# Kernel optimization log

Measured on AMD Instinct MI355X. Metric: run time of the kernel, lower is better.

## Reference

```python
import jax, jax.numpy as jnp
import numpy as np

OUT_H, OUT_W = 7, 7  # output_size from init_kwargs


def setup_inputs() -> dict:
    key = jax.random.key(0)
    k1, k2 = jax.random.split(key)
    B, C, H, W = 2, 256, 200, 304
    N = 512  # proposals per image
    feature_map = jax.random.normal(k1, (B, C, H, W), dtype=jnp.float32)
    u = jax.random.uniform(k2, (B, N, 5), dtype=jnp.float32)
    # [cx, cy, w, h, angle_deg] in image coordinates
    boxes = jnp.stack([
        u[..., 0] * W,            # cx in [0, W)
        u[..., 1] * H,            # cy in [0, H)
        16.0 + u[..., 2] * 100.0, # w in [16, 116)
        16.0 + u[..., 3] * 100.0, # h in [16, 116)
        u[..., 4] * 360.0,        # angle in degrees
    ], axis=-1)
    return {"feature_map": feature_map, "boxes": boxes}


def _make_grid(boxes, H, W):
    # boxes: [B, N, 5] -> normalized sampling grid (gx, gy) each [B, N, OUT_H, OUT_W]
    cx, cy, w, h, ang = (boxes[..., i] for i in range(5))
    rad = -ang * (jnp.pi / 180.0)
    c, s = jnp.cos(rad), jnp.sin(rad)
    a00 = w / W * c
    a01 = -h / H * s
    a02 = 2.0 * cx / W - 1.0
    a10 = w / W * s
    a11 = h / H * c
    a12 = 2.0 * cy / H - 1.0
    # affine_grid base coords, align_corners=False
    xs = (2.0 * jnp.arange(OUT_W, dtype=boxes.dtype) + 1.0) / OUT_W - 1.0  # [OUT_W]
    ys = (2.0 * jnp.arange(OUT_H, dtype=boxes.dtype) + 1.0) / OUT_H - 1.0  # [OUT_H]
    xs = xs[None, None, None, :]
    ys = ys[None, None, :, None]
    gx = a00[..., None, None] * xs + a01[..., None, None] * ys + a02[..., None, None]
    gy = a10[..., None, None] * xs + a11[..., None, None] * ys + a12[..., None, None]
    return gx, gy


def _sample_one_image(fm, ix, iy):
    # fm: [C, H, W]; ix, iy: [N, OUT_H, OUT_W] pixel coords. Bilinear, zero padding.
    H, W = fm.shape[1], fm.shape[2]
    x0 = jnp.floor(ix)
    y0 = jnp.floor(iy)
    wx1 = ix - x0
    wy1 = iy - y0

    def corner(yc, xc, wgt):
        valid = (xc >= 0) & (xc <= W - 1) & (yc >= 0) & (yc <= H - 1)
        xi = jnp.clip(xc, 0, W - 1).astype(jnp.int32)
        yi = jnp.clip(yc, 0, H - 1).astype(jnp.int32)
        vals = fm[:, yi, xi]  # [C, N, OUT_H, OUT_W]
        return vals * (wgt * valid)[None]

    out = (corner(y0, x0, (1 - wy1) * (1 - wx1))
           + corner(y0, x0 + 1, (1 - wy1) * wx1)
           + corner(y0 + 1, x0, wy1 * (1 - wx1))
           + corner(y0 + 1, x0 + 1, wy1 * wx1))
    return jnp.transpose(out, (1, 0, 2, 3))  # [N, C, OUT_H, OUT_W]


def reference(feature_map, boxes):
    B, C, H, W = feature_map.shape
    N = boxes.shape[1]
    gx, gy = _make_grid(boxes, H, W)  # normalized [-1, 1]
    # grid_sample align_corners=False coordinate transform
    ix = ((gx + 1.0) * W - 1.0) * 0.5
    iy = ((gy + 1.0) * H - 1.0) * 0.5
    pooled = jax.vmap(_sample_one_image)(feature_map, ix, iy)  # [B, N, C, OUT_H, OUT_W]
    return pooled.reshape(B * N, C, OUT_H, OUT_W)
```

## Files before the change

kernel.cpp:

```cpp
#include <hip/hip_runtime.h>
#include <hip/hip_fp16.h>

#define B_   2
#define C_   256
#define H_   200
#define W_   304
#define HW_  60800
#define N_   512
#define OH_  7
#define OW_  7
#define POS_ 49
#define CPB_ 12544
#define PD_  258

__global__ __launch_bounds__(256) void transpose_f16_kernel(
    const float* __restrict__ fm,
    __half* __restrict__ fmT)
{
    __shared__ float tile[64 * 65];

    const int blk = blockIdx.x;
    const int b   = blk / 3800;
    const int r   = blk - b * 3800;
    const int hwT = r >> 2;
    const int cT  = r & 3;
    const int hw0 = hwT * 64;
    const int c0  = cT * 64;

    const int t      = threadIdx.x;
    const int lane16 = t & 15;
    const int grp    = t >> 4;

    const float* src = fm + ((size_t)b * C_ + c0) * HW_ + hw0;

    #pragma unroll
    for (int p = 0; p < 4; ++p) {
        const int c_local = p * 16 + grp;
        const float4 v = *(const float4*)(src + (size_t)c_local * HW_ + lane16 * 4);
        float* dl = &tile[c_local * 65 + lane16 * 4];
        dl[0] = v.x; dl[1] = v.y; dl[2] = v.z; dl[3] = v.w;
    }
    __syncthreads();

    __half* dst = fmT + ((size_t)b * HW_ + hw0) * C_ + c0;

    #pragma unroll
    for (int p = 0; p < 4; ++p) {
        const int hw_local = p * 16 + grp;
        ushort4 u;
        u.x = __half_as_ushort(__float2half_rn(tile[(lane16 * 4 + 0) * 65 + hw_local]));
        u.y = __half_as_ushort(__float2half_rn(tile[(lane16 * 4 + 1) * 65 + hw_local]));
        u.z = __half_as_ushort(__float2half_rn(tile[(lane16 * 4 + 2) * 65 + hw_local]));
        u.w = __half_as_ushort(__float2half_rn(tile[(lane16 * 4 + 3) * 65 + hw_local]));
        *(ushort4*)(dst + (size_t)hw_local * C_ + lane16 * 4) = u;
    }
}

__global__ __launch_bounds__(256) void gather_f16_kernel(
    const __half* __restrict__ fmT,
    const float* __restrict__ boxes,
    float* __restrict__ out)
{
    __shared__ int4   sOff[POS_];
    __shared__ float4 sWgt[POS_];
    __shared__ float  sVal[48 * PD_ + 256];

    const int bn  = blockIdx.x;
    const int b   = bn >> 9;
    const int tid = threadIdx.x;

    if (tid < POS_) {
        const float* bx = boxes + (size_t)bn * 5;
        const float cx = bx[0], cy = bx[1], w = bx[2], h = bx[3], ang = bx[4];

        const float rad = -ang * 0.017453292519943295f;
        const float cr = cosf(rad), sr = sinf(rad);

        const float a00 =  w * (1.0f / W_) * cr;
        const float a01 = -h * (1.0f / H_) * sr;
        const float a02 =  2.0f * cx * (1.0f / W_) - 1.0f;
        const float a10 =  w * (1.0f / W_) * sr;
        const float a11 =  h * (1.0f / H_) * cr;
        const float a12 =  2.0f * cy * (1.0f / H_) - 1.0f;

        const int py = tid / OW_;
        const int px = tid - py * OW_;
        const float xs = (2.0f * (float)px + 1.0f) / (float)OW_ - 1.0f;
        const float ys = (2.0f * (float)py + 1.0f) / (float)OH_ - 1.0f;

        const float gx = a00 * xs + a01 * ys + a02;
        const float gy = a10 * xs + a11 * ys + a12;

        const float ix = ((gx + 1.0f) * (float)W_ - 1.0f) * 0.5f;
        const float iy = ((gy + 1.0f) * (float)H_ - 1.0f) * 0.5f;

        const float x0f = floorf(ix), y0f = floorf(iy);
        const float wx1 = ix - x0f,  wy1 = iy - y0f;
        const float wx0 = 1.0f - wx1, wy0 = 1.0f - wy1;
        const float x1f = x0f + 1.0f, y1f = y0f + 1.0f;

        const float vx0 = (x0f >= 0.0f && x0f <= (float)(W_ - 1)) ? 1.0f : 0.0f;
        const float vx1 = (x1f >= 0.0f && x1f <= (float)(W_ - 1)) ? 1.0f : 0.0f;
        const float vy0 = (y0f >= 0.0f && y0f <= (float)(H_ - 1)) ? 1.0f : 0.0f;
        const float vy1 = (y1f >= 0.0f && y1f <= (float)(H_ - 1)) ? 1.0f : 0.0f;

        const int xi0 = (int)fminf(fmaxf(x0f, 0.0f), (float)(W_ - 1));
        const int xi1 = (int)fminf(fmaxf(x1f, 0.0f), (float)(W_ - 1));
        const int yi0 = (int)fminf(fmaxf(y0f, 0.0f), (float)(H_ - 1));
        const int yi1 = (int)fminf(fmaxf(y1f, 0.0f), (float)(H_ - 1));

        sOff[tid] = make_int4((yi0 * W_ + xi0) * C_, (yi0 * W_ + xi1) * C_,
                              (yi1 * W_ + xi0) * C_, (yi1 * W_ + xi1) * C_);
        sWgt[tid] = make_float4(wy0 * wx0 * (vy0 * vx0),
                                wy0 * wx1 * (vy0 * vx1),
                                wy1 * wx0 * (vy1 * vx0),
                                wy1 * wx1 * (vy1 * vx1));
    }
    __syncthreads();

    const int t128 = tid & 127;
    const int pg   = tid >> 7;
    const int c    = t128 * 2;

    const __half* __restrict__ fb = fmT + (size_t)b * HW_ * C_ + c;

    for (int pos = pg; pos < POS_; pos += 2) {
        const int4   o  = sOff[pos];
        const float4 wv = sWgt[pos];

        const float2 f0 = __half22float2(*(const __half2*)(fb + o.x));
        const float2 f1 = __half22float2(*(const __half2*)(fb + o.y));
        const float2 f2 = __half22float2(*(const __half2*)(fb + o.z));
        const float2 f3 = __half22float2(*(const __half2*)(fb + o.w));

        const float vx = wv.x * f0.x + wv.y * f1.x + wv.z * f2.x + wv.w * f3.x;
        const float vy = wv.x * f0.y + wv.y * f1.y + wv.z * f2.y + wv.w * f3.y;

        *(float2*)&sVal[pos * PD_ + c] = make_float2(vx, vy);
    }
    __syncthreads();

    float* __restrict__ ob = out + (size_t)bn * CPB_;

    #pragma unroll 7
    for (int it = 0; it < POS_; ++it) {
        const int flat = it * 256 + tid;
        const int cc   = flat / POS_;
        const int pos  = flat - cc * POS_;
        ob[flat] = sVal[pos * PD_ + cc];
    }
}

__global__ __launch_bounds__(256) void rroi_align_fallback(
    const float* __restrict__ fm,
    const float* __restrict__ boxes,
    float* __restrict__ out)
{
    __shared__ int4   sOff[POS_];
    __shared__ float4 sWgt[POS_];

    const int bn  = blockIdx.x;
    const int b   = bn >> 9;
    const int tid = threadIdx.x;

    if (tid < POS_) {
        const float* bx = boxes + (size_t)bn * 5;
        const float cx = bx[0], cy = bx[1], w = bx[2], h = bx[3], ang = bx[4];
        const float rad = -ang * 0.017453292519943295f;
        const float cr = cosf(rad), sr = sinf(rad);
        const float a00 =  w * (1.0f / W_) * cr;
        const float a01 = -h * (1.0f / H_) * sr;
        const float a02 =  2.0f * cx * (1.0f / W_) - 1.0f;
        const float a10 =  w * (1.0f / W_) * sr;
        const float a11 =  h * (1.0f / H_) * cr;
        const float a12 =  2.0f * cy * (1.0f / H_) - 1.0f;
        const int py = tid / OW_;
        const int px = tid - py * OW_;
        const float xs = (2.0f * (float)px + 1.0f) / (float)OW_ - 1.0f;
        const float ys = (2.0f * (float)py + 1.0f) / (float)OH_ - 1.0f;
        const float gx = a00 * xs + a01 * ys + a02;
        const float gy = a10 * xs + a11 * ys + a12;
        const float ix = ((gx + 1.0f) * (float)W_ - 1.0f) * 0.5f;
        const float iy = ((gy + 1.0f) * (float)H_ - 1.0f) * 0.5f;
        const float x0f = floorf(ix), y0f = floorf(iy);
        const float wx1 = ix - x0f,  wy1 = iy - y0f;
        const float wx0 = 1.0f - wx1, wy0 = 1.0f - wy1;
        const float x1f = x0f + 1.0f, y1f = y0f + 1.0f;
        const float vx0 = (x0f >= 0.0f && x0f <= (float)(W_ - 1)) ? 1.0f : 0.0f;
        const float vx1 = (x1f >= 0.0f && x1f <= (float)(W_ - 1)) ? 1.0f : 0.0f;
        const float vy0 = (y0f >= 0.0f && y0f <= (float)(H_ - 1)) ? 1.0f : 0.0f;
        const float vy1 = (y1f >= 0.0f && y1f <= (float)(H_ - 1)) ? 1.0f : 0.0f;
        const int xi0 = (int)fminf(fmaxf(x0f, 0.0f), (float)(W_ - 1));
        const int xi1 = (int)fminf(fmaxf(x1f, 0.0f), (float)(W_ - 1));
        const int yi0 = (int)fminf(fmaxf(y0f, 0.0f), (float)(H_ - 1));
        const int yi1 = (int)fminf(fmaxf(y1f, 0.0f), (float)(H_ - 1));
        sOff[tid] = make_int4(yi0 * W_ + xi0, yi0 * W_ + xi1,
                              yi1 * W_ + xi0, yi1 * W_ + xi1);
        sWgt[tid] = make_float4(wy0 * wx0 * (vy0 * vx0),
                                wy0 * wx1 * (vy0 * vx1),
                                wy1 * wx0 * (vy1 * vx0),
                                wy1 * wx1 * (vy1 * vx1));
    }
    __syncthreads();

    const float* __restrict__ fb = fm + (size_t)b * C_ * HW_;
    float* __restrict__ ob = out + (size_t)bn * CPB_;

    #pragma unroll 7
    for (int it = 0; it < POS_; ++it) {
        const int flat = it * 256 + tid;
        const int cc   = flat / POS_;
        const int pos  = flat - cc * POS_;
        const int4   o  = sOff[pos];
        const float4 wv = sWgt[pos];
        const float* __restrict__ plane = fb + (size_t)cc * HW_;
        ob[flat] = wv.x * plane[o.x] + wv.y * plane[o.y]
                 + wv.z * plane[o.z] + wv.w * plane[o.w];
    }
}

extern "C" void kernel_launch(void* const* d_in, const int* in_sizes, int n_in,
                              void* d_out, int out_size, void* d_ws, size_t ws_size,
                              hipStream_t stream) {
    const float* fm    = (const float*)d_in[0];
    const float* boxes = (const float*)d_in[1];
    float* out         = (float*)d_out;

    const size_t needed = (size_t)B_ * C_ * HW_ * sizeof(__half);

    if (ws_size >= needed) {
        __half* fmT = (__half*)d_ws;
        transpose_f16_kernel<<<dim3(2 * 950 * 4), dim3(256), 0, stream>>>(fm, fmT);
        gather_f16_kernel<<<dim3(B_ * N_), dim3(256), 0, stream>>>(fmT, boxes, out);
    } else {
        rroi_align_fallback<<<dim3(B_ * N_), dim3(256), 0, stream>>>(fm, boxes, out);
    }
}
```

Measured before the change: 226.4 us.

## Widen transpose tiles to full channels and vectorize fp16 gather with half staging

The transpose kernel now has each block cover 64 spatial positions across all 256 channels, converting to fp16 in registers before staging in a ushort shared tile, then writing 16-byte rows. The gather kernel loads four fp16 channels per thread, stages the interpolated results as fp16 in shared memory, and writes the output as float4. The goal is fewer, wider global transactions and smaller shared-memory footprint. The cost is an extra fp16 rounding of the interpolated values, which reduces accuracy, and more scalar divides in the output loop.

After: 222.6 us. About the same (-1.7%).

```diff
diff --git a/kernel.cpp b/kernel.cpp
--- a/kernel.cpp
+++ b/kernel.cpp
@@ -11,59 +11,77 @@
 #define OW_  7
 #define POS_ 49
 #define CPB_ 12544
-#define PD_  258
-
-__global__ __launch_bounds__(256) void transpose_f16_kernel(
+
+#define TP_PITCH 260
+#define GP_PITCH 264
+
+__global__ __launch_bounds__(256) void transpose_f16_v3(
     const float* __restrict__ fm,
-    __half* __restrict__ fmT)
+    ushort* __restrict__ fmT)
 {
-    __shared__ float tile[64 * 65];
+    __shared__ ushort tile[64 * TP_PITCH];
 
     const int blk = blockIdx.x;
-    const int b   = blk / 3800;
-    const int r   = blk - b * 3800;
-    const int hwT = r >> 2;
-    const int cT  = r & 3;
+    const int b   = blk / 950;
+    const int hwT = blk - b * 950;
     const int hw0 = hwT * 64;
-    const int c0  = cT * 64;
-
-    const int t      = threadIdx.x;
-    const int lane16 = t & 15;
-    const int grp    = t >> 4;
-
-    const float* src = fm + ((size_t)b * C_ + c0) * HW_ + hw0;
-
+
+    const int t = threadIdx.x;
+
+    const float* __restrict__ src = fm + (size_t)b * C_ * HW_ + hw0;
+
+    float4 r[4][4];
     #pragma unroll
-    for (int p = 0; p < 4; ++p) {
-        const int c_local = p * 16 + grp;
-        const float4 v = *(const float4*)(src + (size_t)c_local * HW_ + lane16 * 4);
-        float* dl = &tile[c_local * 65 + lane16 * 4];
-        dl[0] = v.x; dl[1] = v.y; dl[2] = v.z; dl[3] = v.w;
+    for (int i = 0; i < 4; ++i) {
+        const int p  = i * 256 + t;
+        const int cq = p >> 4;
+        const int hq = p & 15;
+        #pragma unroll
+        for (int j = 0; j < 4; ++j) {
+            r[i][j] = *(const float4*)(src + (size_t)(cq * 4 + j) * HW_ + hq * 4);
+        }
+    }
+
+    #pragma unroll
+    for (int i = 0; i < 4; ++i) {
+        const int p  = i * 256 + t;
+        const int cq = p >> 4;
+        const int hq = p & 15;
+        #pragma unroll
+        for (int j2 = 0; j2 < 4; ++j2) {
+            ushort4 u;
+            u.x = __half_as_ushort(__float2half_rn(((const float*)&r[i][0])[j2]));
+            u.y = __half_as_ushort(__float2half_rn(((const float*)&r[i][1])[j2]));
+            u.z = __half_as_ushort(__float2half_rn(((const float*)&r[i][2])[j2]));
+            u.w = __half_as_ushort(__float2half_rn(((const float*)&r[i][3])[j2]));
+            *(ushort4*)&tile[(hq * 4 + j2) * TP_PITCH + cq * 4] = u;
+        }
     }
     __syncthreads();
 
-    __half* dst = fmT + ((size_t)b * HW_ + hw0) * C_ + c0;
+    ushort* __restrict__ dst = fmT + ((size_t)b * HW_ + hw0) * C_;
+    const int lane32 = t & 31;
+    const int rsub   = t >> 5;
 
     #pragma unroll
-    for (int p = 0; p < 4; ++p) {
-        const int hw_local = p * 16 + grp;
-        ushort4 u;
-        u.x = __half_as_ushort(__float2half_rn(tile[(lane16 * 4 + 0) * 65 + hw_local]));
-        u.y = __half_as_ushort(__float2half_rn(tile[(lane16 * 4 + 1) * 65 + hw_local]));
-        u.z = __half_as_ushort(__float2half_rn(tile[(lane16 * 4 + 2) * 65 + hw_local]));
-        u.w = __half_as_ushort(__float2half_rn(tile[(lane16 * 4 + 3) * 65 + hw_local]));
-        *(ushort4*)(dst + (size_t)hw_local * C_ + lane16 * 4) = u;
+    for (int k = 0; k < 8; ++k) {
+        const int row = k * 8 + rsub;
+        const ushort* sp = &tile[row * TP_PITCH + lane32 * 8];
+        const uint2 lo = *(const uint2*)(sp);
+        const uint2 hi = *(const uint2*)(sp + 4);
+        uint4 v; v.x = lo.x; v.y = lo.y; v.z = hi.x; v.w = hi.y;
+        *(uint4*)(dst + (size_t)row * C_ + lane32 * 8) = v;
     }
 }
 
-__global__ __launch_bounds__(256) void gather_f16_kernel(
-    const __half* __restrict__ fmT,
+__global__ __launch_bounds__(256) void gather_f16_v2(
+    const ushort* __restrict__ fmT,
     const float* __restrict__ boxes,
     float* __restrict__ out)
 {
     __shared__ int4   sOff[POS_];
     __shared__ float4 sWgt[POS_];
-    __shared__ float  sVal[48 * PD_ + 256];
+    __shared__ ushort sVal[POS_ * GP_PITCH];
 
     const int bn  = blockIdx.x;
     const int b   = bn >> 9;
@@ -118,36 +136,80 @@
     }
     __syncthreads();
 
-    const int t128 = tid & 127;
-    const int pg   = tid >> 7;
-    const int c    = t128 * 2;
-
-    const __half* __restrict__ fb = fmT + (size_t)b * HW_ * C_ + c;
-
-    for (int pos = pg; pos < POS_; pos += 2) {
+    const int lane = tid & 63;
+    const int pg   = tid >> 6;
+    const int c    = lane * 4;
+
+    const ushort* __restrict__ fb = fmT + (size_t)b * HW_ * C_ + c;
+
+    for (int pos = pg; pos < POS_; pos += 4) {
         const int4   o  = sOff[pos];
         const float4 wv = sWgt[pos];
 
-        const float2 f0 = __half22float2(*(const __half2*)(fb + o.x));
-        const float2 f1 = __half22float2(*(const __half2*)(fb + o.y));
-        const float2 f2 = __half22float2(*(const __half2*)(fb + o.z));
-        const float2 f3 = __half22float2(*(const __half2*)(fb + o.w));
-
-        const float vx = wv.x * f0.x + wv.y * f1.x + wv.z * f2.x + wv.w * f3.x;
-        const float vy = wv.x * f0.y + wv.y * f1.y + wv.z * f2.y + wv.w * f3.y;
-
-        *(float2*)&sVal[pos * PD_ + c] = make_float2(vx, vy);
+        const ushort4 q0 = *(const ushort4*)(fb + o.x);
+        const ushort4 q1 = *(const ushort4*)(fb + o.y);
+        const ushort4 q2 = *(const ushort4*)(fb + o.z);
+        const ushort4 q3 = *(const ushort4*)(fb + o.w);
+
+        ushort4 u;
+        {
+            const float a = wv.x * __half2float(__ushort_as_half(q0.x))
+                          + wv.y * __half2float(__ushort_as_half(q1.x))
+                          + wv.z * __half2float(__ushort_as_half(q2.x))
+                          + wv.w * __half2float(__ushort_as_half(q3.x));
+            u.x = __half_as_ushort(__float2half_rn(a));
+        }
+        {
+            const float a = wv.x * __half2float(__ushort_as_half(q0.y))
+                          + wv.y * __half2float(__ushort_as_half(q1.y))
+                          + wv.z * __half2float(__ushort_as_half(q2.y))
+                          + wv.w * __half2float(__ushort_as_half(q3.y));
+            u.y = __half_as_ushort(__float2half_rn(a));
+        }
+        {
+            const float a = wv.x * __half2float(__ushort_as_half(q0.z))
+                          + wv.y * __half2float(__ushort_as_half(q1.z))
+                          + wv.z * __half2float(__ushort_as_half(q2.z))
+                          + wv.w * __half2float(__ushort_as_half(q3.z));
+            u.z = __half_as_ushort(__float2half_rn(a));
+        }
+        {
+            const float a = wv.x * __half2float(__ushort_as_half(q0.w))
+                          + wv.y * __half2float(__ushort_as_half(q1.w))
+                          + wv.z * __half2float(__ushort_as_half(q2.w))
+                          + wv.w * __half2float(__ushort_as_half(q3.w));
+            u.w = __half_as_ushort(__float2half_rn(a));
+        }
+        *(ushort4*)&sVal[pos * GP_PITCH + c] = u;
     }
     __syncthreads();
 
     float* __restrict__ ob = out + (size_t)bn * CPB_;
 
-    #pragma unroll 7
-    for (int it = 0; it < POS_; ++it) {
-        const int flat = it * 256 + tid;
-        const int cc   = flat / POS_;
-        const int pos  = flat - cc * POS_;
-        ob[flat] = sVal[pos * PD_ + cc];
+    #pragma unroll
+    for (int it = 0; it < 13; ++it) {
+        const int flat4 = it * 256 + tid;
+        if (flat4 < 3136) {
+            const int base = flat4 * 4;
+            float4 v;
+            {
+                const int f = base + 0; const int cc = f / POS_; const int pp = f - cc * POS_;
+                v.x = __half2float(__ushort_as_half(sVal[pp * GP_PITCH + cc]));
+            }
+            {
+                const int f = base + 1; const int cc = f / POS_; const int pp = f - cc * POS_;
+                v.y = __half2float(__ushort_as_half(sVal[pp * GP_PITCH + cc]));
+            }
+            {
+                const int f = base + 2; const int cc = f / POS_; const int pp = f - cc * POS_;
+                v.z = __half2float(__ushort_as_half(sVal[pp * GP_PITCH + cc]));
+            }
+            {
+                const int f = base + 3; const int cc = f / POS_; const int pp = f - cc * POS_;
+                v.w = __half2float(__ushort_as_half(sVal[pp * GP_PITCH + cc]));
+            }
+            *(float4*)(ob + base) = v;
+        }
     }
 }
 
@@ -226,12 +288,12 @@
     const float* boxes = (const float*)d_in[1];
     float* out         = (float*)d_out;
 
-    const size_t needed = (size_t)B_ * C_ * HW_ * sizeof(__half);
+    const size_t needed = (size_t)B_ * C_ * HW_ * sizeof(ushort);
 
     if (ws_size >= needed) {
-        __half* fmT = (__half*)d_ws;
-        transpose_f16_kernel<<<dim3(2 * 950 * 4), dim3(256), 0, stream>>>(fm, fmT);
-        gather_f16_kernel<<<dim3(B_ * N_), dim3(256), 0, stream>>>(fmT, boxes, out);
+        ushort* fmT = (ushort*)d_ws;
+        transpose_f16_v3<<<dim3(2 * 950), dim3(256), 0, stream>>>(fm, fmT);
+        gather_f16_v2<<<dim3(B_ * N_), dim3(256), 0, stream>>>(fmT, boxes, out);
     } else {
         rroi_align_fallback<<<dim3(B_ * N_), dim3(256), 0, stream>>>(fm, boxes, out);
     }
```
